# Performance work log

Measured on AMD Instinct MI355X. Metric: run time of the kernel, lower is better.

Reference implementation:

```python
import jax, jax.numpy as jnp
import numpy as np

PRIOR = 0.1      # prior_prob
P_NOISE = 0.05   # p
DAMPING = 0.5
BETA = 0.3
EPS = 1e-10


def compute_likelihood(Y_edges, prod_fail_others, beta_edges, p):
    p_sick_if_healthy = 1.0 - prod_fail_others
    p_sick_if_infected = 1.0 - prod_fail_others * (1.0 - beta_edges)
    normal_if_sick = (1.0 - p) * p_sick_if_healthy
    sick_if_sick = (1.0 - p) * p_sick_if_infected
    normal_if_normal = p * p_sick_if_healthy + (1.0 - p_sick_if_healthy)
    sick_if_normal = p * p_sick_if_infected + (1.0 - p_sick_if_infected)
    is_pos = Y_edges == 1
    L0 = jnp.where(is_pos, normal_if_sick, normal_if_normal)
    L1 = jnp.where(is_pos, sick_if_sick, sick_if_normal)
    return L0, L1


def setup_inputs() -> dict:
    key = jax.random.key(0)
    k1, k2, k3 = jax.random.split(key, 3)
    num_tests = 100000
    num_patients = 200000
    num_edges = 12800000
    Y_obs = jax.random.randint(k1, (num_tests,), 0, 2, dtype=jnp.int32)
    idx_i = jax.random.randint(k2, (num_edges,), 0, num_tests, dtype=jnp.int32)
    idx_j = jax.random.randint(k3, (num_edges,), 0, num_patients, dtype=jnp.int32)
    # beta_edges = 1.0 on diagonal entries, beta elsewhere (as in __init__)
    beta_edges = jnp.where(idx_i == idx_j, 1.0, BETA).astype(jnp.float32)
    return {"Y_obs": Y_obs, "idx_i": idx_i, "idx_j": idx_j,
            "beta_edges": beta_edges, "max_iters": 50,
            "num_patients": num_patients}


def reference(Y_obs, idx_i, idx_j, beta_edges, max_iters, num_patients):
    num_tests = Y_obs.shape[0]
    num_edges = idx_i.shape[0]
    Y_edges = Y_obs[idx_i]  # [E]

    def step(carry, it):
        msg_j_to_i, old0, old1, _ = carry
        # test-side aggregation: prob all other patients failed to infect test i
        fail = 1.0 - beta_edges * msg_j_to_i
        log_fail = jnp.log(fail + EPS)
        tot_log_fail = jax.ops.segment_sum(log_fail, idx_i, num_segments=num_tests)
        prod_fail_others = jnp.exp(tot_log_fail[idx_i]) / (fail + EPS)
        new0, new1 = compute_likelihood(Y_edges, prod_fail_others, beta_edges, P_NOISE)
        first = it == 0
        m0 = jnp.where(first, new0, DAMPING * new0 + (1.0 - DAMPING) * old0)
        m1 = jnp.where(first, new1, DAMPING * new1 + (1.0 - DAMPING) * old1)
        old0_n, old1_n = m0, m1  # stored BEFORE normalization, as in torch code
        norm = m0 + m1 + EPS
        log_m0 = jnp.log(m0 / norm + EPS)
        log_m1 = jnp.log(m1 / norm + EPS)
        # patient-side aggregation
        t0 = jax.ops.segment_sum(log_m0, idx_j, num_segments=num_patients)
        t1 = jax.ops.segment_sum(log_m1, idx_j, num_segments=num_patients)
        log_b0 = jnp.log(1.0 - PRIOR) + t0
        log_b1 = jnp.log(PRIOR) + t1
        beliefs = jax.nn.sigmoid(log_b1 - log_b0)  # = 1/(1+exp(lb0-lb1))
        msg_next = jax.nn.sigmoid((log_b1[idx_j] - log_m1) - (log_b0[idx_j] - log_m0))
        return (msg_next, old0_n, old1_n, beliefs), None

    init = (jnp.full((num_edges,), PRIOR, dtype=jnp.float32),
            jnp.zeros((num_edges,), jnp.float32),
            jnp.zeros((num_edges,), jnp.float32),
            jnp.full((num_patients,), PRIOR, dtype=jnp.float32))
    (_, _, _, node_beliefs), _ = jax.lax.scan(step, init, jnp.arange(max_iters))
    return node_beliefs
```

## Files before the change

### kernel.cpp

```cpp
#include <hip/hip_runtime.h>
#include <hip/hip_fp16.h>

#define EPSF   1e-10f
#define PRIORF 0.1f
#define QF     0.95f
#define BETAF  0.3f
#define BS     256
#define WPB    4
#define CAPT   4
#define LOGIT_PRIOR (-2.1972245773362196f)
#define GSH    13
#define NG_MAX 32
#define SPAN_I 256
#define NB2_MAX 1024
#define SPAN_J 128
#define NBJ_MAX 2048
#define CHA    16384
#define CHJ    32768
#define D16    0x2000u
#define JL16   0x1FFFu
#define NXCD   8
#define BLK_SL 2048

__device__ __forceinline__ float wave_sum(float v) {
    #pragma unroll
    for (int m = 32; m >= 1; m >>= 1) v += __shfl_xor(v, m, 64);
    return v;
}
__device__ __forceinline__ float frcp(float x) {
    return __builtin_amdgcn_rcpf(x);
}
__device__ __forceinline__ float calcD(float2 o) {
    float inv = frcp(o.x + o.y + EPSF);
    return __logf(o.y * inv + EPSF) - __logf(o.x * inv + EPSF);
}
__device__ __forceinline__ float sigmoidf(float x) {
    return frcp(1.0f + __expf(-x));
}
__device__ __forceinline__ float2 unpack(__half2 h) {
    return make_float2(__low2float(h), __high2float(h));
}

__device__ __forceinline__ int run_search(int cum, int len, int v0,
                                          int cidx, int NG, int* gout) {
    int lo = 0, hi = NG - 1;
    #pragma unroll
    for (int st = 0; st < 5; ++st) {
        int mid = (lo + hi) >> 1;
        int cmid = __shfl(cum, mid);
        int open = (lo < hi);
        int p = (cmid > cidx);
        int nhi = p ? mid : hi;
        int nlo = p ? lo : (mid + 1);
        hi = open ? nhi : hi;
        lo = open ? nlo : lo;
    }
    int cl = __shfl(cum, lo);
    int ll = __shfl(len, lo);
    int vv = __shfl(v0, lo);
    *gout = lo;
    return vv + cidx - (cl - ll);
}

__global__ __launch_bounds__(BS) void k_test(
    const int*            __restrict__ rowptrG,
    const unsigned short* __restrict__ jidx16,
    const int*            __restrict__ Y,
    const float*          __restrict__ delta,
    __half2*              __restrict__ oldm,
    int T, int NG, int first)
{
    int lane = threadIdx.x & 63;
    int i = blockIdx.x * WPB + (threadIdx.x >> 6);
    if (i >= T) return;
    int v0 = 0, v1 = 0;
    if (lane < NG) v0 = rowptrG[(size_t)i * NG + lane];
    int l2 = lane - 32;
    if (l2 >= 0 && l2 < NG) v1 = rowptrG[(size_t)(i + 1) * NG + l2];
    int endv = __shfl(v1, 32 + lane);
    int len = (lane < NG) ? (endv - v0) : 0;
    int cum = len;
    #pragma unroll
    for (int off = 1; off < 64; off <<= 1) {
        int t = __shfl_up(cum, off);
        if (lane >= off) cum += t;
    }
    int deg = __shfl(cum, 63);
    int nch = (deg + 63) >> 6;
    int ypos = (Y[i] == 1);
    float lsum = 0.0f;

    if (deg <= 64 * CAPT) {
        int ssv[CAPT]; int ksv[CAPT]; float2 osv[CAPT]; float fsv[CAPT];
        #pragma unroll
        for (int c = 0; c < CAPT; ++c) {
            if (c >= nch) break;
            int idx = c * 64 + lane;
            int cidx = min(idx, deg - 1);
            int g;
            int s = run_search(cum, len, v0, cidx, NG, &g);
            bool act = (idx < deg);
            int k = 0; float2 o = make_float2(0.f, 0.f); float f = 1.0f;
            if (act) {
                k = jidx16[s];
                float b = (k & D16) ? 1.0f : BETAF;
                float msg;
                if (first) msg = PRIORF;
                else {
                    o = unpack(oldm[s]);
                    int j = (g << GSH) | (k & JL16);
                    msg = sigmoidf(delta[j] - calcD(o));
                }
                f = 1.0f - b * msg;
                lsum += __logf(f + EPSF);
            }
            ssv[c] = act ? s : -1; ksv[c] = k; osv[c] = o; fsv[c] = f;
        }
        float Etot = __expf(wave_sum(lsum));
        #pragma unroll
        for (int c = 0; c < CAPT; ++c) {
            if (c >= nch) break;
            int s = ssv[c];
            if (s < 0) continue;
            int k = ksv[c]; float f = fsv[c];
            float b = (k & D16) ? 1.0f : BETAF;
            float prod = Etot * frcp(f + EPSF);
            float psh = 1.0f - prod;
            float psi = 1.0f - prod * (1.0f - b);
            float L0 = ypos ? QF * psh : 1.0f - QF * psh;
            float L1 = ypos ? QF * psi : 1.0f - QF * psi;
            float m0, m1;
            if (first) { m0 = L0; m1 = L1; }
            else { float2 o = osv[c]; m0 = 0.5f * L0 + 0.5f * o.x;
                                      m1 = 0.5f * L1 + 0.5f * o.y; }
            oldm[s] = __floats2half2_rn(m0, m1);
        }
    } else {
        for (int base = 0; base < deg; base += 64) {
            int idx = base + lane;
            int cidx = min(idx, deg - 1);
            int g;
            int s = run_search(cum, len, v0, cidx, NG, &g);
            if (idx < deg) {
                int k = jidx16[s];
                float b = (k & D16) ? 1.0f : BETAF;
                float msg;
                if (first) msg = PRIORF;
                else {
                    int j = (g << GSH) | (k & JL16);
                    msg = sigmoidf(delta[j] - calcD(unpack(oldm[s])));
                }
                lsum += __logf(1.0f - b * msg + EPSF);
            }
        }
        float Etot = __expf(wave_sum(lsum));
        for (int base = 0; base < deg; base += 64) {
            int idx = base + lane;
            int cidx = min(idx, deg - 1);
            int g;
            int s = run_search(cum, len, v0, cidx, NG, &g);
            if (idx < deg) {
                int k = jidx16[s];
                float b = (k & D16) ? 1.0f : BETAF;
                float2 o = make_float2(0.f, 0.f);
                float msg;
                if (first) msg = PRIORF;
                else { o = unpack(oldm[s]);
                       int j = (g << GSH) | (k & JL16);
                       msg = sigmoidf(delta[j] - calcD(o)); }
                float f = 1.0f - b * msg;
                float prod = Etot * frcp(f + EPSF);
                float psh = 1.0f - prod;
                float psi = 1.0f - prod * (1.0f - b);
                float L0 = ypos ? QF * psh : 1.0f - QF * psh;
                float L1 = ypos ? QF * psi : 1.0f - QF * psi;
                float m0, m1;
                if (first) { m0 = L0; m1 = L1; }
                else { m0 = 0.5f * L0 + 0.5f * o.x; m1 = 0.5f * L1 + 0.5f * o.y; }
                oldm[s] = __floats2half2_rn(m0, m1);
            }
        }
    }
}

__global__ __launch_bounds__(BS) void k_patient(
    const int*     __restrict__ colptr,
    const int*     __restrict__ eposJ,
    const __half2* __restrict__ oldm,
    float*         __restrict__ delta,
    float*         __restrict__ out, int P, int NG)
{
    int b = blockIdx.x;
    int x = b & (NXCD - 1);
    int r = b >> 3;
    int m = r / BLK_SL;
    int w = r % BLK_SL;
    int g = x + NXCD * m;
    if (g >= NG) return;
    int lane = threadIdx.x & 63;
    int p = (g << GSH) + w * WPB + (threadIdx.x >> 6);
    if (p >= P) return;
    int u0 = colptr[p], u1 = colptr[p + 1];
    float S = 0.0f;
    for (int u = u0 + lane; u < u1; u += 64)
        S += calcD(unpack(oldm[eposJ[u]]));
    S = wave_sum(S);
    if (lane == 0) {
        float d = LOGIT_PRIOR + S;
        delta[p] = d;
        out[p] = sigmoidf(d);
    }
}

__global__ void k_zf2(int* frontG, int* front2, int* frontJ,
                      int NG, int nb2tot, int nbj) {
    int t = blockIdx.x * blockDim.x + threadIdx.x;
    if (t <= NG) frontG[t] = 0;
    if (t <= nb2tot) front2[t] = 0;
    if (t <= nbj) frontJ[t] = 0;
}

__global__ __launch_bounds__(BS) void k_binG(
    const int* __restrict__ idx_i, const int* __restrict__ idx_j,
    int* __restrict__ frontG, unsigned* __restrict__ stageA,
    int E, int NG, int capA)
{
    __shared__ int h[NG_MAX], rsv[NG_MAX], cu[NG_MAX];
    int tid = threadIdx.x;
    if (tid < NG) h[tid] = 0;
    __syncthreads();
    int start = blockIdx.x * CHA, end = min(start + CHA, E);
    for (int e = start + tid; e < end; e += BS)
        atomicAdd(&h[idx_j[e] >> GSH], 1);
    __syncthreads();
    if (tid < NG) { int c = h[tid];
        rsv[tid] = c ? atomicAdd(&frontG[tid], c) : 0; cu[tid] = 0; }
    __syncthreads();
    for (int e = start + tid; e < end; e += BS) {
        int i = idx_i[e], j = idx_j[e];
        int g = j >> GSH;
        int pos = rsv[g] + atomicAdd(&cu[g], 1);
        if (pos < capA)
            stageA[(size_t)g * capA + pos] =
                ((unsigned)i << 14) | ((unsigned)(i == j) << 13)
                | (unsigned)(j & ((1 << GSH) - 1));
    }
}

__global__ __launch_bounds__(BS) void k_binI2(
    const unsigned* __restrict__ stageA, const int* __restrict__ frontG,
    int* __restrict__ front2, unsigned* __restrict__ stage2,
    int NG, int NB2, int capA, int cap2, int chunks)
{
    int g = blockIdx.x / chunks, c = blockIdx.x % chunks;
    int n = min(frontG[g], capA);
    int start = c * 2 * CHA, end = min(start + 2 * CHA, n);
    if (start >= end) return;
    __shared__ int h[NB2_MAX], rsv[NB2_MAX], cu[NB2_MAX];
    int tid = threadIdx.x;
    for (int b = tid; b < NB2; b += BS) h[b] = 0;
    __syncthreads();
    const unsigned* rb = stageA + (size_t)g * capA;
    for (int r = start + tid; r < end; r += BS)
        atomicAdd(&h[(rb[r] >> 14) >> 8], 1);
    __syncthreads();
    for (int b = tid; b < NB2; b += BS) {
        int cc = h[b];
        rsv[b] = cc ? atomicAdd(&front2[g * NB2 + b], cc) : 0;
        cu[b] = 0;
    }
    __syncthreads();
    for (int r = start + tid; r < end; r += BS) {
        unsigned v = rb[r];
        int i = (int)(v >> 14);
        int ib = i >> 8;
        int pos = rsv[ib] + atomicAdd(&cu[ib], 1);
        if (pos < cap2)
            stage2[(size_t)(g * NB2 + ib) * cap2 + pos] =
                ((unsigned)(i & 255) << 14) | (v & 0x3FFFu);
    }
}

__global__ void k_scan_front(int* a, int n, int cap) {
    __shared__ int tmp[BS];
    __shared__ int carry;
    int tid = threadIdx.x;
    if (tid == 0) carry = 0;
    __syncthreads();
    for (int base = 0; base < n; base += BS) {
        int i = base + tid;
        int v = (i < n) ? min(a[i], cap) : 0;
        tmp[tid] = v; __syncthreads();
        for (int off = 1; off < BS; off <<= 1) {
            int x = (tid >= off) ? tmp[tid - off] : 0;
            __syncthreads();
            tmp[tid] += x;
            __syncthreads();
        }
        int c = carry;
        if (i < n) a[i] = c + tmp[tid] - v;
        __syncthreads();
        if (tid == BS - 1) carry = c + tmp[tid];
        __syncthreads();
    }
    if (tid == 0) a[n] = carry;
}

__global__ __launch_bounds__(BS) void k_csr2(
    const unsigned* __restrict__ stage2, const int* __restrict__ front2s,
    int* __restrict__ rowptrG, unsigned short* __restrict__ jidx16,
    int T, int NG, int NB2, int cap2)
{
    __shared__ int deg[SPAN_I], loff[SPAN_I], cu[SPAN_I];
    int b = blockIdx.x, tid = threadIdx.x;
    int g = b / NB2, ib = b % NB2;
    int base = front2s[b];
    int n = min(front2s[b + 1] - base, cap2);
    deg[tid] = 0;
    __syncthreads();
    const unsigned* rb = stage2 + (size_t)b * cap2;
    for (int r = tid; r < n; r += BS)
        atomicAdd(&deg[rb[r] >> 14], 1);
    __syncthreads();
    loff[tid] = deg[tid];
    __syncthreads();
    for (int off = 1; off < SPAN_I; off <<= 1) {
        int v = (tid >= off) ? loff[tid - off] : 0;
        __syncthreads();
        loff[tid] += v;
        __syncthreads();
    }
    {
        int excl = loff[tid] - deg[tid];
        int i = ib * SPAN_I + tid;
        if (i < T) rowptrG[(size_t)i * NG + g] = base + excl;
        cu[tid] = base + excl;
    }
    __syncthreads();
    for (int r = tid; r < n; r += BS) {
        unsigned v = rb[r];
        int pos = atomicAdd(&cu[v >> 14], 1);
        jidx16[pos] = (unsigned short)(v & 0x3FFFu);
    }
}

__global__ void k_fin(const int* front2s, int* rowptrG, int T, int NG, int NB2) {
    int g = threadIdx.x;
    if (g < NG) rowptrG[(size_t)T * NG + g] = front2s[(g + 1) * NB2];
}

__global__ __launch_bounds__(BS) void k_binJ(
    const unsigned short* __restrict__ jidx16,
    const int* __restrict__ front2s,
    int* __restrict__ front, unsigned int* __restrict__ stage,
    int E, int nbj, int cap, int NG, int NB2)
{
    __shared__ int h[NBJ_MAX], rsv[NBJ_MAX], cu[NBJ_MAX];
    __shared__ int ends[NG_MAX];
    int tid = threadIdx.x;
    if (tid < NG) ends[tid] = front2s[(tid + 1) * NB2];
    for (int b = tid; b < nbj; b += BS) h[b] = 0;
    __syncthreads();
    int start = blockIdx.x * CHJ, end = min(start + CHJ, E);
    for (int e = start + tid; e < end; e += BS) {
        int lo = 0, hi = NG - 1;
        while (lo < hi) { int mid = (lo + hi) >> 1;
                          if (e < ends[mid]) hi = mid; else lo = mid + 1; }
        int j = (lo << GSH) | (jidx16[e] & JL16);
        atomicAdd(&h[j >> 7], 1);
    }
    __syncthreads();
    for (int b = tid; b < nbj; b += BS) {
        int c = h[b];
        rsv[b] = c ? atomicAdd(&front[b], c) : 0;
        cu[b] = 0;
    }
    __syncthreads();
    for (int e = start + tid; e < end; e += BS) {
        int lo = 0, hi = NG - 1;
        while (lo < hi) { int mid = (lo + hi) >> 1;
                          if (e < ends[mid]) hi = mid; else lo = mid + 1; }
        int j = (lo << GSH) | (jidx16[e] & JL16);
        int bb = j >> 7;
        int pos = rsv[bb] + atomicAdd(&cu[bb], 1);
        if (pos < cap)
            stage[(size_t)bb * cap + pos] = ((unsigned)(j & 127) << 24) | (unsigned)e;
    }
}

__global__ __launch_bounds__(BS) void k_csrJ(
    const unsigned int* __restrict__ stage, const int* __restrict__ fbase,
    int* __restrict__ colptr, int* __restrict__ eposJ, int P, int E, int cap)
{
    __shared__ int deg[SPAN_J], loff[SPAN_J], cu[SPAN_J];
    int b = blockIdx.x, tid = threadIdx.x;
    int gbase = fbase[b];
    int n = min(fbase[b + 1] - gbase, cap);
    if (tid < SPAN_J) deg[tid] = 0;
    __syncthreads();
    const unsigned int* rb = stage + (size_t)b * cap;
    for (int r = tid; r < n; r += BS)
        atomicAdd(&deg[rb[r] >> 24], 1);
    __syncthreads();
    if (tid < SPAN_J) loff[tid] = deg[tid];
    __syncthreads();
    for (int off = 1; off < SPAN_J; off <<= 1) {
        int v = 0;
        if (tid < SPAN_J && tid >= off) v = loff[tid - off];
        __syncthreads();
        if (tid < SPAN_J) loff[tid] += v;
        __syncthreads();
    }
    if (tid < SPAN_J) {
        int excl = loff[tid] - deg[tid];
        int p = b * SPAN_J + tid;
        if (p < P) colptr[p] = gbase + excl;
        cu[tid] = gbase + excl;
    }
    __syncthreads();
    for (int r = tid; r < n; r += BS) {
        unsigned int v = rb[r];
        int pos = atomicAdd(&cu[v >> 24], 1);
        eposJ[pos] = (int)(v & 0xFFFFFFu);
    }
    if (b == 0 && tid == 0) colptr[P] = E;
}

extern "C" void kernel_launch(void* const* d_in, const int* in_sizes, int n_in,
                              void* d_out, int out_size, void* d_ws, size_t ws_size,
                              hipStream_t stream) {
    const int* Y     = (const int*)d_in[0];
    const int* idx_i = (const int*)d_in[1];
    const int* idx_j = (const int*)d_in[2];
    const int T = in_sizes[0];
    const int E = in_sizes[1];
    const int P = out_size;
    const int ITERS = 50;

    int* eposJ = (int*)d_in[3];

    const int NG     = (P + (1 << GSH) - 1) >> GSH;
    const int NB2    = (T + SPAN_I - 1) / SPAN_I;
    const int nb2tot = NG * NB2;
    const int nbj    = (P + SPAN_J - 1) / SPAN_J;
    long long meanA = (long long)E * (1 << GSH) / P;
    const int capA  = (int)(meanA + (meanA >> 6) + 4096);
    long long mean2 = meanA * SPAN_I / T;
    const int cap2  = (int)(mean2 + (mean2 >> 4) + 256);
    const int capJ  = E / nbj + E / (nbj * 8) + 1024;

    char* ws = (char*)d_ws;
    auto alloc = [&](size_t bytes) -> char* {
        char* p = ws; ws += (bytes + 255) & ~(size_t)255; return p;
    };
    int* rowptrG = (int*)alloc((size_t)(T + 1) * NG * 4);
    int* colptr  = (int*)alloc((size_t)(P + 1) * 4);
    int* frontG  = (int*)alloc((size_t)(NG + 1) * 4);
    int* front2  = (int*)alloc((size_t)(nb2tot + 1) * 4);
    int* frontJ  = (int*)alloc((size_t)(nbj + 1) * 4);
    size_t szA = (size_t)capA * NG * 4, szjx = (size_t)E * 2;
    char* regionA = alloc(szA > szjx ? szA : szjx);
    unsigned*       stageA = (unsigned*)regionA;
    unsigned short* jidx16 = (unsigned short*)regionA;
    size_t oldm_b = ((size_t)E * 4 + 255) & ~(size_t)255;
    size_t sz2 = (size_t)cap2 * nb2tot * 4;
    size_t szJ = (size_t)capJ * nbj * 4;
    size_t szO = oldm_b + (size_t)P * 4;
    size_t szB = sz2 > szJ ? sz2 : szJ; if (szO > szB) szB = szO;
    char* regionB = alloc(szB);
    unsigned* stage2 = (unsigned*)regionB;
    unsigned* stageJ = (unsigned*)regionB;
    __half2*  oldm   = (__half2*)regionB;
    float*    delta  = (float*)(regionB + oldm_b);
    float*    out    = (float*)d_out;

    const int zb = (nb2tot + BS) / BS + 1;
    const int chunks = (capA + 2 * CHA - 1) / (2 * CHA);
    k_zf2<<<zb, BS, 0, stream>>>(frontG, front2, frontJ, NG, nb2tot, nbj);
    k_binG<<<(E + CHA - 1) / CHA, BS, 0, stream>>>(idx_i, idx_j, frontG, stageA,
                                                   E, NG, capA);
    k_binI2<<<NG * chunks, BS, 0, stream>>>(stageA, frontG, front2, stage2,
                                            NG, NB2, capA, cap2, chunks);
    k_scan_front<<<1, BS, 0, stream>>>(front2, nb2tot, cap2);
    k_csr2<<<nb2tot, BS, 0, stream>>>(stage2, front2, rowptrG, jidx16,
                                      T, NG, NB2, cap2);
    k_fin<<<1, 64, 0, stream>>>(front2, rowptrG, T, NG, NB2);
    k_binJ<<<(E + CHJ - 1) / CHJ, BS, 0, stream>>>(jidx16, front2, frontJ, stageJ,
                                                   E, nbj, capJ, NG, NB2);
    k_scan_front<<<1, BS, 0, stream>>>(frontJ, nbj, capJ);
    k_csrJ<<<nbj, BS, 0, stream>>>(stageJ, frontJ, colptr, eposJ, P, E, capJ);

    const int tgrid = (T + WPB - 1) / WPB;
    const int maxm  = (NG + NXCD - 1) / NXCD;
    const int pgrid = NXCD * maxm * BLK_SL;
    for (int it = 0; it < ITERS; ++it) {
        k_test<<<tgrid, BS, 0, stream>>>(rowptrG, jidx16, Y, delta, oldm,
                                         T, NG, it == 0);
        k_patient<<<pgrid, BS, 0, stream>>>(colptr, eposJ, oldm, delta, out,
                                            P, NG);
    }
}
```

Before: 9.546 ms.

## Precompute compact per-test edge streams to drop per-iteration run search

Adds a one-time preprocessing pass that builds a compact per-test row pointer and two edge streams. One stream packs the group and edge slot, the other holds the 16-bit patient index. The test kernel then reads these streams directly instead of rebuilding offsets from a per-group rowptr with a wave scan and binary search every iteration. The patient kernel moves to 1024-thread blocks with 16 waves each, and a binning chunk size is reduced. The cost is extra preprocessing kernels, about 6 bytes of stream storage per edge, and a workspace layout that reuses overlapping buffers.

```diff
diff --git a/kernel.cpp b/kernel.cpp
--- a/kernel.cpp
+++ b/kernel.cpp
@@ -16,11 +16,13 @@
 #define SPAN_J 128
 #define NBJ_MAX 2048
 #define CHA    16384
-#define CHJ    32768
+#define CHJ    8192
 #define D16    0x2000u
 #define JL16   0x1FFFu
 #define NXCD   8
-#define BLK_SL 2048
+#define BSP    1024
+#define WPBP   16
+#define BLK_SLP 512
 
 __device__ __forceinline__ float wave_sum(float v) {
     #pragma unroll
@@ -30,15 +32,15 @@
 __device__ __forceinline__ float frcp(float x) {
     return __builtin_amdgcn_rcpf(x);
 }
+__device__ __forceinline__ float2 unpack(__half2 h) {
+    return make_float2(__low2float(h), __high2float(h));
+}
 __device__ __forceinline__ float calcD(float2 o) {
     float inv = frcp(o.x + o.y + EPSF);
     return __logf(o.y * inv + EPSF) - __logf(o.x * inv + EPSF);
 }
 __device__ __forceinline__ float sigmoidf(float x) {
     return frcp(1.0f + __expf(-x));
-}
-__device__ __forceinline__ float2 unpack(__half2 h) {
-    return make_float2(__low2float(h), __high2float(h));
 }
 
 __device__ __forceinline__ int run_search(int cum, int len, int v0,
@@ -63,12 +65,332 @@
 }
 
 __global__ __launch_bounds__(BS) void k_test(
-    const int*            __restrict__ rowptrG,
-    const unsigned short* __restrict__ jidx16,
+    const int*            __restrict__ rowptrC,
+    const unsigned*       __restrict__ strmA,
+    const unsigned short* __restrict__ strmB,
     const int*            __restrict__ Y,
     const float*          __restrict__ delta,
     __half2*              __restrict__ oldm,
-    int T, int NG, int first)
+    int T, int first)
+{
+    int lane = threadIdx.x & 63;
+    int i = blockIdx.x * WPB + (threadIdx.x >> 6);
+    if (i >= T) return;
+    int r0 = rowptrC[i];
+    int deg = rowptrC[i + 1] - r0;
+    int nch = (deg + 63) >> 6;
+    int ypos = (Y[i] == 1);
+    float lsum = 0.0f;
+
+    if (deg <= 64 * CAPT) {
+        unsigned av[CAPT]; int kv[CAPT]; float2 ov[CAPT]; float fv[CAPT];
+        #pragma unroll
+        for (int c = 0; c < CAPT; ++c) {
+            if (c >= nch) break;
+            int idx = c * 64 + lane;
+            int q = r0 + min(idx, deg - 1);
+            unsigned a = strmA[q];
+            int k = strmB[q];
+            bool act = (idx < deg);
+            float2 o = make_float2(0.f, 0.f);
+            float b = (k & D16) ? 1.0f : BETAF;
+            float msg;
+            if (first) msg = PRIORF;
+            else {
+                int s = (int)(a & 0xFFFFFFu);
+                o = unpack(oldm[s]);
+                int j = ((int)(a >> 24) << GSH) | (k & JL16);
+                msg = sigmoidf(delta[j] - calcD(o));
+            }
+            float f = 1.0f - b * msg;
+            if (act) lsum += __logf(f + EPSF);
+            av[c] = a; kv[c] = k; ov[c] = o; fv[c] = f;
+        }
+        float Etot = __expf(wave_sum(lsum));
+        #pragma unroll
+        for (int c = 0; c < CAPT; ++c) {
+            if (c >= nch) break;
+            int idx = c * 64 + lane;
+            if (idx >= deg) continue;
+            int k = kv[c]; float f = fv[c];
+            float b = (k & D16) ? 1.0f : BETAF;
+            float prod = Etot * frcp(f + EPSF);
+            float psh = 1.0f - prod;
+            float psi = 1.0f - prod * (1.0f - b);
+            float L0 = ypos ? QF * psh : 1.0f - QF * psh;
+            float L1 = ypos ? QF * psi : 1.0f - QF * psi;
+            float m0, m1;
+            if (first) { m0 = L0; m1 = L1; }
+            else { m0 = 0.5f * L0 + 0.5f * ov[c].x;
+                   m1 = 0.5f * L1 + 0.5f * ov[c].y; }
+            int s = (int)(av[c] & 0xFFFFFFu);
+            oldm[s] = __floats2half2_rn(m0, m1);
+        }
+    } else {
+        for (int base = 0; base < deg; base += 64) {
+            int idx = base + lane;
+            int q = r0 + min(idx, deg - 1);
+            unsigned a = strmA[q];
+            int k = strmB[q];
+            float b = (k & D16) ? 1.0f : BETAF;
+            float msg;
+            if (first) msg = PRIORF;
+            else {
+                int s = (int)(a & 0xFFFFFFu);
+                int j = ((int)(a >> 24) << GSH) | (k & JL16);
+                msg = sigmoidf(delta[j] - calcD(unpack(oldm[s])));
+            }
+            if (idx < deg) lsum += __logf(1.0f - b * msg + EPSF);
+        }
+        float Etot = __expf(wave_sum(lsum));
+        for (int base = 0; base < deg; base += 64) {
+            int idx = base + lane;
+            int q = r0 + min(idx, deg - 1);
+            unsigned a = strmA[q];
+            int k = strmB[q];
+            float b = (k & D16) ? 1.0f : BETAF;
+            int s = (int)(a & 0xFFFFFFu);
+            float2 o = make_float2(0.f, 0.f);
+            float msg;
+            if (first) msg = PRIORF;
+            else {
+                o = unpack(oldm[s]);
+                int j = ((int)(a >> 24) << GSH) | (k & JL16);
+                msg = sigmoidf(delta[j] - calcD(o));
+            }
+            float f = 1.0f - b * msg;
+            float prod = Etot * frcp(f + EPSF);
+            float psh = 1.0f - prod;
+            float psi = 1.0f - prod * (1.0f - b);
+            float L0 = ypos ? QF * psh : 1.0f - QF * psh;
+            float L1 = ypos ? QF * psi : 1.0f - QF * psi;
+            float m0, m1;
+            if (first) { m0 = L0; m1 = L1; }
+            else { m0 = 0.5f * L0 + 0.5f * o.x; m1 = 0.5f * L1 + 0.5f * o.y; }
+            if (idx < deg) oldm[s] = __floats2half2_rn(m0, m1);
+        }
+    }
+}
+
+__global__ __launch_bounds__(BSP) void k_patient(
+    const int*     __restrict__ colptr,
+    const int*     __restrict__ eposJ,
+    const __half2* __restrict__ oldm,
+    float*         __restrict__ delta,
+    float*         __restrict__ out, int P, int NG)
+{
+    int b = blockIdx.x;
+    int x = b & (NXCD - 1);
+    int r = b >> 3;
+    int m = r >> 9;
+    int w = r & (BLK_SLP - 1);
+    int g = x + NXCD * m;
+    if (g >= NG) return;
+    int lane = threadIdx.x & 63;
+    int p = (g << GSH) + w * WPBP + (threadIdx.x >> 6);
+    if (p >= P) return;
+    int u0 = colptr[p], u1 = colptr[p + 1];
+    float S = 0.0f;
+    for (int u = u0 + lane; u < u1; u += 64)
+        S += calcD(unpack(oldm[eposJ[u]]));
+    S = wave_sum(S);
+    if (lane == 0) {
+        float d = LOGIT_PRIOR + S;
+        delta[p] = d;
+        out[p] = sigmoidf(d);
+    }
+}
+
+__global__ void k_zf2(int* frontG, int* front2, int* frontJ,
+                      int NG, int nb2tot, int nbj) {
+    int t = blockIdx.x * blockDim.x + threadIdx.x;
+    if (t <= NG) frontG[t] = 0;
+    if (t <= nb2tot) front2[t] = 0;
+    if (t <= nbj) frontJ[t] = 0;
+}
+
+__global__ __launch_bounds__(BS) void k_binG(
+    const int* __restrict__ idx_i, const int* __restrict__ idx_j,
+    int* __restrict__ frontG, unsigned* __restrict__ stageA,
+    int E, int NG, int capA)
+{
+    __shared__ int h[NG_MAX], rsv[NG_MAX], cu[NG_MAX];
+    int tid = threadIdx.x;
+    if (tid < NG) h[tid] = 0;
+    __syncthreads();
+    int start = blockIdx.x * CHA, end = min(start + CHA, E);
+    for (int e = start + tid; e < end; e += BS)
+        atomicAdd(&h[idx_j[e] >> GSH], 1);
+    __syncthreads();
+    if (tid < NG) { int c = h[tid];
+        rsv[tid] = c ? atomicAdd(&frontG[tid], c) : 0; cu[tid] = 0; }
+    __syncthreads();
+    for (int e = start + tid; e < end; e += BS) {
+        int i = idx_i[e], j = idx_j[e];
+        int g = j >> GSH;
+        int pos = rsv[g] + atomicAdd(&cu[g], 1);
+        if (pos < capA)
+            stageA[(size_t)g * capA + pos] =
+                ((unsigned)i << 14) | ((unsigned)(i == j) << 13)
+                | (unsigned)(j & ((1 << GSH) - 1));
+    }
+}
+
+__global__ __launch_bounds__(BS) void k_binI2(
+    const unsigned* __restrict__ stageA, const int* __restrict__ frontG,
+    int* __restrict__ front2, unsigned* __restrict__ stage2,
+    int NG, int NB2, int capA, int cap2, int chunks)
+{
+    int g = blockIdx.x / chunks, c = blockIdx.x % chunks;
+    int n = min(frontG[g], capA);
+    int start = c * 2 * CHA, end = min(start + 2 * CHA, n);
+    if (start >= end) return;
+    __shared__ int h[NB2_MAX], rsv[NB2_MAX], cu[NB2_MAX];
+    int tid = threadIdx.x;
+    for (int b = tid; b < NB2; b += BS) h[b] = 0;
+    __syncthreads();
+    const unsigned* rb = stageA + (size_t)g * capA;
+    for (int r = start + tid; r < end; r += BS)
+        atomicAdd(&h[(rb[r] >> 14) >> 8], 1);
+    __syncthreads();
+    for (int b = tid; b < NB2; b += BS) {
+        int cc = h[b];
+        rsv[b] = cc ? atomicAdd(&front2[g * NB2 + b], cc) : 0;
+        cu[b] = 0;
+    }
+    __syncthreads();
+    for (int r = start + tid; r < end; r += BS) {
+        unsigned v = rb[r];
+        int i = (int)(v >> 14);
+        int ib = i >> 8;
+        int pos = rsv[ib] + atomicAdd(&cu[ib], 1);
+        if (pos < cap2)
+            stage2[(size_t)(g * NB2 + ib) * cap2 + pos] =
+                ((unsigned)(i & 255) << 14) | (v & 0x3FFFu);
+    }
+}
+
+__global__ void k_scan_front(int* a, int n, int cap) {
+    __shared__ int tmp[BS];
+    __shared__ int carry;
+    int tid = threadIdx.x;
+    if (tid == 0) carry = 0;
+    __syncthreads();
+    for (int base = 0; base < n; base += BS) {
+        int i = base + tid;
+        int v = (i < n) ? min(a[i], cap) : 0;
+        tmp[tid] = v; __syncthreads();
+        for (int off = 1; off < BS; off <<= 1) {
+            int x = (tid >= off) ? tmp[tid - off] : 0;
+            __syncthreads();
+            tmp[tid] += x;
+            __syncthreads();
+        }
+        int c = carry;
+        if (i < n) a[i] = c + tmp[tid] - v;
+        __syncthreads();
+        if (tid == BS - 1) carry = c + tmp[tid];
+        __syncthreads();
+    }
+    if (tid == 0) a[n] = carry;
+}
+
+__global__ __launch_bounds__(BS) void k_csr2(
+    const unsigned* __restrict__ stage2, const int* __restrict__ front2s,
+    int* __restrict__ rowptrG, unsigned short* __restrict__ jidx16,
+    int T, int NG, int NB2, int cap2)
+{
+    __shared__ int deg[SPAN_I], loff[SPAN_I], cu[SPAN_I];
+    int b = blockIdx.x, tid = threadIdx.x;
+    int g = b / NB2, ib = b % NB2;
+    int base = front2s[b];
+    int n = min(front2s[b + 1] - base, cap2);
+    deg[tid] = 0;
+    __syncthreads();
+    const unsigned* rb = stage2 + (size_t)b * cap2;
+    for (int r = tid; r < n; r += BS)
+        atomicAdd(&deg[rb[r] >> 14], 1);
+    __syncthreads();
+    loff[tid] = deg[tid];
+    __syncthreads();
+    for (int off = 1; off < SPAN_I; off <<= 1) {
+        int v = (tid >= off) ? loff[tid - off] : 0;
+        __syncthreads();
+        loff[tid] += v;
+        __syncthreads();
+    }
+    {
+        int excl = loff[tid] - deg[tid];
+        int i = ib * SPAN_I + tid;
+        if (i < T) rowptrG[(size_t)i * NG + g] = base + excl;
+        cu[tid] = base + excl;
+    }
+    __syncthreads();
+    for (int r = tid; r < n; r += BS) {
+        unsigned v = rb[r];
+        int pos = atomicAdd(&cu[v >> 14], 1);
+        jidx16[pos] = (unsigned short)(v & 0x3FFFu);
+    }
+}
+
+__global__ void k_fin(const int* front2s, int* rowptrG, int T, int NG, int NB2) {
+    int g = threadIdx.x;
+    if (g < NG) rowptrG[(size_t)T * NG + g] = front2s[(g + 1) * NB2];
+}
+
+__global__ __launch_bounds__(BS) void k_degrow(
+    const int* __restrict__ rowptrG, int* __restrict__ cnt, int T, int NG)
+{
+    int i = blockIdx.x * BS + threadIdx.x;
+    if (i >= T) return;
+    int d = 0;
+    for (int g = 0; g < NG; ++g)
+        d += rowptrG[(size_t)(i + 1) * NG + g] - rowptrG[(size_t)i * NG + g];
+    cnt[i] = d;
+}
+
+__global__ __launch_bounds__(BS) void k_scan_part(
+    const int* __restrict__ in, int* __restrict__ aux, int n)
+{
+    __shared__ int t[BS];
+    int b = blockIdx.x, tid = threadIdx.x;
+    int i = b * BS + tid;
+    int v = (i < n) ? in[i] : 0;
+    t[tid] = v; __syncthreads();
+    for (int off = 1; off < BS; off <<= 1) {
+        int x = (tid >= off) ? t[tid - off] : 0;
+        __syncthreads();
+        t[tid] += x;
+        __syncthreads();
+    }
+    if (tid == BS - 1) aux[b] = t[tid];
+}
+__global__ __launch_bounds__(BS) void k_scan_fin(
+    const int* __restrict__ in, const int* __restrict__ aux,
+    int* __restrict__ out, int n, int nblk)
+{
+    __shared__ int t[BS];
+    int b = blockIdx.x, tid = threadIdx.x;
+    int i = b * BS + tid;
+    int v = (i < n) ? in[i] : 0;
+    t[tid] = v; __syncthreads();
+    for (int off = 1; off < BS; off <<= 1) {
+        int x = (tid >= off) ? t[tid - off] : 0;
+        __syncthreads();
+        t[tid] += x;
+        __syncthreads();
+    }
+    if (i < n) out[i] = aux[b] + t[tid] - v;
+    if (b == 0 && tid == 0) out[n] = aux[nblk];
+}
+
+__global__ __launch_bounds__(BS) void k_mkrow(
+    const int*            __restrict__ rowptrG,
+    const unsigned short* __restrict__ jidx16,
+    const int*            __restrict__ rowptrC,
+    unsigned*             __restrict__ strmA,
+    unsigned short*       __restrict__ strmB,
+    int T, int NG)
 {
     int lane = threadIdx.x & 63;
     int i = blockIdx.x * WPB + (threadIdx.x >> 6);
@@ -86,267 +408,18 @@
         if (lane >= off) cum += t;
     }
     int deg = __shfl(cum, 63);
-    int nch = (deg + 63) >> 6;
-    int ypos = (Y[i] == 1);
-    float lsum = 0.0f;
-
-    if (deg <= 64 * CAPT) {
-        int ssv[CAPT]; int ksv[CAPT]; float2 osv[CAPT]; float fsv[CAPT];
-        #pragma unroll
-        for (int c = 0; c < CAPT; ++c) {
-            if (c >= nch) break;
-            int idx = c * 64 + lane;
-            int cidx = min(idx, deg - 1);
-            int g;
-            int s = run_search(cum, len, v0, cidx, NG, &g);
-            bool act = (idx < deg);
-            int k = 0; float2 o = make_float2(0.f, 0.f); float f = 1.0f;
-            if (act) {
-                k = jidx16[s];
-                float b = (k & D16) ? 1.0f : BETAF;
-                float msg;
-                if (first) msg = PRIORF;
-                else {
-                    o = unpack(oldm[s]);
-                    int j = (g << GSH) | (k & JL16);
-                    msg = sigmoidf(delta[j] - calcD(o));
-                }
-                f = 1.0f - b * msg;
-                lsum += __logf(f + EPSF);
-            }
-            ssv[c] = act ? s : -1; ksv[c] = k; osv[c] = o; fsv[c] = f;
+    int r0 = rowptrC[i];
+    for (int base = 0; base < deg; base += 64) {
+        int idx = base + lane;
+        int cidx = min(idx, deg - 1);
+        int g;
+        int s = run_search(cum, len, v0, cidx, NG, &g);
+        if (idx < deg) {
+            int q = r0 + idx;
+            strmA[q] = ((unsigned)g << 24) | (unsigned)s;
+            strmB[q] = jidx16[s];
         }
-        float Etot = __expf(wave_sum(lsum));
-        #pragma unroll
-        for (int c = 0; c < CAPT; ++c) {
-            if (c >= nch) break;
-            int s = ssv[c];
-            if (s < 0) continue;
-            int k = ksv[c]; float f = fsv[c];
-            float b = (k & D16) ? 1.0f : BETAF;
-            float prod = Etot * frcp(f + EPSF);
-            float psh = 1.0f - prod;
-            float psi = 1.0f - prod * (1.0f - b);
-            float L0 = ypos ? QF * psh : 1.0f - QF * psh;
-            float L1 = ypos ? QF * psi : 1.0f - QF * psi;
-            float m0, m1;
-            if (first) { m0 = L0; m1 = L1; }
-            else { float2 o = osv[c]; m0 = 0.5f * L0 + 0.5f * o.x;
-                                      m1 = 0.5f * L1 + 0.5f * o.y; }
-            oldm[s] = __floats2half2_rn(m0, m1);
-        }
-    } else {
-        for (int base = 0; base < deg; base += 64) {
-            int idx = base + lane;
-            int cidx = min(idx, deg - 1);
-            int g;
-            int s = run_search(cum, len, v0, cidx, NG, &g);
-            if (idx < deg) {
-                int k = jidx16[s];
-                float b = (k & D16) ? 1.0f : BETAF;
-                float msg;
-                if (first) msg = PRIORF;
-                else {
-                    int j = (g << GSH) | (k & JL16);
-                    msg = sigmoidf(delta[j] - calcD(unpack(oldm[s])));
-                }
-                lsum += __logf(1.0f - b * msg + EPSF);
-            }
-        }
-        float Etot = __expf(wave_sum(lsum));
-        for (int base = 0; base < deg; base += 64) {
-            int idx = base + lane;
-            int cidx = min(idx, deg - 1);
-            int g;
-            int s = run_search(cum, len, v0, cidx, NG, &g);
-            if (idx < deg) {
-                int k = jidx16[s];
-                float b = (k & D16) ? 1.0f : BETAF;
-                float2 o = make_float2(0.f, 0.f);
-                float msg;
-                if (first) msg = PRIORF;
-                else { o = unpack(oldm[s]);
-                       int j = (g << GSH) | (k & JL16);
-                       msg = sigmoidf(delta[j] - calcD(o)); }
-                float f = 1.0f - b * msg;
-                float prod = Etot * frcp(f + EPSF);
-                float psh = 1.0f - prod;
-                float psi = 1.0f - prod * (1.0f - b);
-                float L0 = ypos ? QF * psh : 1.0f - QF * psh;
-                float L1 = ypos ? QF * psi : 1.0f - QF * psi;
-                float m0, m1;
-                if (first) { m0 = L0; m1 = L1; }
-                else { m0 = 0.5f * L0 + 0.5f * o.x; m1 = 0.5f * L1 + 0.5f * o.y; }
-                oldm[s] = __floats2half2_rn(m0, m1);
-            }
-        }
-    }
-}
-
-__global__ __launch_bounds__(BS) void k_patient(
-    const int*     __restrict__ colptr,
-    const int*     __restrict__ eposJ,
-    const __half2* __restrict__ oldm,
-    float*         __restrict__ delta,
-    float*         __restrict__ out, int P, int NG)
-{
-    int b = blockIdx.x;
-    int x = b & (NXCD - 1);
-    int r = b >> 3;
-    int m = r / BLK_SL;
-    int w = r % BLK_SL;
-    int g = x + NXCD * m;
-    if (g >= NG) return;
-    int lane = threadIdx.x & 63;
-    int p = (g << GSH) + w * WPB + (threadIdx.x >> 6);
-    if (p >= P) return;
-    int u0 = colptr[p], u1 = colptr[p + 1];
-    float S = 0.0f;
-    for (int u = u0 + lane; u < u1; u += 64)
-        S += calcD(unpack(oldm[eposJ[u]]));
-    S = wave_sum(S);
-    if (lane == 0) {
-        float d = LOGIT_PRIOR + S;
-        delta[p] = d;
-        out[p] = sigmoidf(d);
-    }
-}
-
-__global__ void k_zf2(int* frontG, int* front2, int* frontJ,
-                      int NG, int nb2tot, int nbj) {
-    int t = blockIdx.x * blockDim.x + threadIdx.x;
-    if (t <= NG) frontG[t] = 0;
-    if (t <= nb2tot) front2[t] = 0;
-    if (t <= nbj) frontJ[t] = 0;
-}
-
-__global__ __launch_bounds__(BS) void k_binG(
-    const int* __restrict__ idx_i, const int* __restrict__ idx_j,
-    int* __restrict__ frontG, unsigned* __restrict__ stageA,
-    int E, int NG, int capA)
-{
-    __shared__ int h[NG_MAX], rsv[NG_MAX], cu[NG_MAX];
-    int tid = threadIdx.x;
-    if (tid < NG) h[tid] = 0;
-    __syncthreads();
-    int start = blockIdx.x * CHA, end = min(start + CHA, E);
-    for (int e = start + tid; e < end; e += BS)
-        atomicAdd(&h[idx_j[e] >> GSH], 1);
-    __syncthreads();
-    if (tid < NG) { int c = h[tid];
-        rsv[tid] = c ? atomicAdd(&frontG[tid], c) : 0; cu[tid] = 0; }
-    __syncthreads();
-    for (int e = start + tid; e < end; e += BS) {
-        int i = idx_i[e], j = idx_j[e];
-        int g = j >> GSH;
-        int pos = rsv[g] + atomicAdd(&cu[g], 1);
-        if (pos < capA)
-            stageA[(size_t)g * capA + pos] =
-                ((unsigned)i << 14) | ((unsigned)(i == j) << 13)
-                | (unsigned)(j & ((1 << GSH) - 1));
-    }
-}
-
-__global__ __launch_bounds__(BS) void k_binI2(
-    const unsigned* __restrict__ stageA, const int* __restrict__ frontG,
-    int* __restrict__ front2, unsigned* __restrict__ stage2,
-    int NG, int NB2, int capA, int cap2, int chunks)
-{
-    int g = blockIdx.x / chunks, c = blockIdx.x % chunks;
-    int n = min(frontG[g], capA);
-    int start = c * 2 * CHA, end = min(start + 2 * CHA, n);
-    if (start >= end) return;
-    __shared__ int h[NB2_MAX], rsv[NB2_MAX], cu[NB2_MAX];
-    int tid = threadIdx.x;
-    for (int b = tid; b < NB2; b += BS) h[b] = 0;
-    __syncthreads();
-    const unsigned* rb = stageA + (size_t)g * capA;
-    for (int r = start + tid; r < end; r += BS)
-        atomicAdd(&h[(rb[r] >> 14) >> 8], 1);
-    __syncthreads();
-    for (int b = tid; b < NB2; b += BS) {
-        int cc = h[b];
-        rsv[b] = cc ? atomicAdd(&front2[g * NB2 + b], cc) : 0;
-        cu[b] = 0;
-    }
-    __syncthreads();
-    for (int r = start + tid; r < end; r += BS) {
-        unsigned v = rb[r];
-        int i = (int)(v >> 14);
-        int ib = i >> 8;
-        int pos = rsv[ib] + atomicAdd(&cu[ib], 1);
-        if (pos < cap2)
-            stage2[(size_t)(g * NB2 + ib) * cap2 + pos] =
-                ((unsigned)(i & 255) << 14) | (v & 0x3FFFu);
-    }
-}
-
-__global__ void k_scan_front(int* a, int n, int cap) {
-    __shared__ int tmp[BS];
-    __shared__ int carry;
-    int tid = threadIdx.x;
-    if (tid == 0) carry = 0;
-    __syncthreads();
-    for (int base = 0; base < n; base += BS) {
-        int i = base + tid;
-        int v = (i < n) ? min(a[i], cap) : 0;
-        tmp[tid] = v; __syncthreads();
-        for (int off = 1; off < BS; off <<= 1) {
-            int x = (tid >= off) ? tmp[tid - off] : 0;
-            __syncthreads();
-            tmp[tid] += x;
-            __syncthreads();
-        }
-        int c = carry;
-        if (i < n) a[i] = c + tmp[tid] - v;
-        __syncthreads();
-        if (tid == BS - 1) carry = c + tmp[tid];
-        __syncthreads();
-    }
-    if (tid == 0) a[n] = carry;
-}
-
-__global__ __launch_bounds__(BS) void k_csr2(
-    const unsigned* __restrict__ stage2, const int* __restrict__ front2s,
-    int* __restrict__ rowptrG, unsigned short* __restrict__ jidx16,
-    int T, int NG, int NB2, int cap2)
-{
-    __shared__ int deg[SPAN_I], loff[SPAN_I], cu[SPAN_I];
-    int b = blockIdx.x, tid = threadIdx.x;
-    int g = b / NB2, ib = b % NB2;
-    int base = front2s[b];
-    int n = min(front2s[b + 1] - base, cap2);
-    deg[tid] = 0;
-    __syncthreads();
-    const unsigned* rb = stage2 + (size_t)b * cap2;
-    for (int r = tid; r < n; r += BS)
-        atomicAdd(&deg[rb[r] >> 14], 1);
-    __syncthreads();
-    loff[tid] = deg[tid];
-    __syncthreads();
-    for (int off = 1; off < SPAN_I; off <<= 1) {
-        int v = (tid >= off) ? loff[tid - off] : 0;
-        __syncthreads();
-        loff[tid] += v;
-        __syncthreads();
-    }
-    {
-        int excl = loff[tid] - deg[tid];
-        int i = ib * SPAN_I + tid;
-        if (i < T) rowptrG[(size_t)i * NG + g] = base + excl;
-        cu[tid] = base + excl;
-    }
-    __syncthreads();
-    for (int r = tid; r < n; r += BS) {
-        unsigned v = rb[r];
-        int pos = atomicAdd(&cu[v >> 14], 1);
-        jidx16[pos] = (unsigned short)(v & 0x3FFFu);
-    }
-}
-
-__global__ void k_fin(const int* front2s, int* rowptrG, int T, int NG, int NB2) {
-    int g = threadIdx.x;
-    if (g < NG) rowptrG[(size_t)T * NG + g] = front2s[(g + 1) * NB2];
+    }
 }
 
 __global__ __launch_bounds__(BS) void k_binJ(
@@ -443,36 +516,36 @@
     const int NB2    = (T + SPAN_I - 1) / SPAN_I;
     const int nb2tot = NG * NB2;
     const int nbj    = (P + SPAN_J - 1) / SPAN_J;
+    const int NBLK   = (T + BS - 1) / BS;
     long long meanA = (long long)E * (1 << GSH) / P;
     const int capA  = (int)(meanA + (meanA >> 6) + 4096);
     long long mean2 = meanA * SPAN_I / T;
     const int cap2  = (int)(mean2 + (mean2 >> 4) + 256);
     const int capJ  = E / nbj + E / (nbj * 8) + 1024;
 
-    char* ws = (char*)d_ws;
-    auto alloc = [&](size_t bytes) -> char* {
-        char* p = ws; ws += (bytes + 255) & ~(size_t)255; return p;
+    char* base = (char*)d_ws;
+    size_t sz2 = (size_t)cap2 * nb2tot * 4;
+    unsigned*       strmA  = (unsigned*)base;
+    unsigned short* strmB  = (unsigned short*)(base + (size_t)E * 4);
+    __half2*        oldm   = (__half2*)(base + (size_t)E * 6);
+    unsigned*       stage2 = (unsigned*)base;
+    unsigned*       stageA = (unsigned*)(base + ((sz2 + 255) & ~(size_t)255));
+    unsigned short* jidx16 = (unsigned short*)(base + (size_t)E * 6);
+    int*            rowptrG= (int*)(base + (size_t)E * 8);
+    unsigned*       stageJ = (unsigned*)base;
+    size_t o = (size_t)E * 10;
+    auto sub = [&](size_t bytes) -> char* {
+        char* p = base + o; o += (bytes + 255) & ~(size_t)255; return p;
     };
-    int* rowptrG = (int*)alloc((size_t)(T + 1) * NG * 4);
-    int* colptr  = (int*)alloc((size_t)(P + 1) * 4);
-    int* frontG  = (int*)alloc((size_t)(NG + 1) * 4);
-    int* front2  = (int*)alloc((size_t)(nb2tot + 1) * 4);
-    int* frontJ  = (int*)alloc((size_t)(nbj + 1) * 4);
-    size_t szA = (size_t)capA * NG * 4, szjx = (size_t)E * 2;
-    char* regionA = alloc(szA > szjx ? szA : szjx);
-    unsigned*       stageA = (unsigned*)regionA;
-    unsigned short* jidx16 = (unsigned short*)regionA;
-    size_t oldm_b = ((size_t)E * 4 + 255) & ~(size_t)255;
-    size_t sz2 = (size_t)cap2 * nb2tot * 4;
-    size_t szJ = (size_t)capJ * nbj * 4;
-    size_t szO = oldm_b + (size_t)P * 4;
-    size_t szB = sz2 > szJ ? sz2 : szJ; if (szO > szB) szB = szO;
-    char* regionB = alloc(szB);
-    unsigned* stage2 = (unsigned*)regionB;
-    unsigned* stageJ = (unsigned*)regionB;
-    __half2*  oldm   = (__half2*)regionB;
-    float*    delta  = (float*)(regionB + oldm_b);
-    float*    out    = (float*)d_out;
+    int*   colptr  = (int*)sub((size_t)(P + 1) * 4);
+    int*   rowptrC = (int*)sub((size_t)(T + 1) * 4);
+    float* delta   = (float*)sub((size_t)P * 4);
+    int*   cnt     = (int*)sub((size_t)T * 4);
+    int*   auxS    = (int*)sub((size_t)(NBLK + 2) * 4);
+    int*   frontG  = (int*)sub((size_t)(NG + 1) * 4);
+    int*   front2  = (int*)sub((size_t)(nb2tot + 1) * 4);
+    int*   frontJ  = (int*)sub((size_t)(nbj + 1) * 4);
+    float* out     = (float*)d_out;
 
     const int zb = (nb2tot + BS) / BS + 1;
     const int chunks = (capA + 2 * CHA - 1) / (2 * CHA);
@@ -485,18 +558,24 @@
     k_csr2<<<nb2tot, BS, 0, stream>>>(stage2, front2, rowptrG, jidx16,
                                       T, NG, NB2, cap2);
     k_fin<<<1, 64, 0, stream>>>(front2, rowptrG, T, NG, NB2);
+    k_degrow<<<NBLK, BS, 0, stream>>>(rowptrG, cnt, T, NG);
+    k_scan_part<<<NBLK, BS, 0, stream>>>(cnt, auxS, T);
+    k_scan_front<<<1, BS, 0, stream>>>(auxS, NBLK, 0x7FFFFFFF);
+    k_scan_fin<<<NBLK, BS, 0, stream>>>(cnt, auxS, rowptrC, T, NBLK);
     k_binJ<<<(E + CHJ - 1) / CHJ, BS, 0, stream>>>(jidx16, front2, frontJ, stageJ,
                                                    E, nbj, capJ, NG, NB2);
     k_scan_front<<<1, BS, 0, stream>>>(frontJ, nbj, capJ);
     k_csrJ<<<nbj, BS, 0, stream>>>(stageJ, frontJ, colptr, eposJ, P, E, capJ);
-
     const int tgrid = (T + WPB - 1) / WPB;
+    k_mkrow<<<tgrid, BS, 0, stream>>>(rowptrG, jidx16, rowptrC, strmA, strmB,
+                                      T, NG);
+
     const int maxm  = (NG + NXCD - 1) / NXCD;
-    const int pgrid = NXCD * maxm * BLK_SL;
+    const int pgrid = NXCD * maxm * BLK_SLP;
     for (int it = 0; it < ITERS; ++it) {
-        k_test<<<tgrid, BS, 0, stream>>>(rowptrG, jidx16, Y, delta, oldm,
-                                         T, NG, it == 0);
-        k_patient<<<pgrid, BS, 0, stream>>>(colptr, eposJ, oldm, delta, out,
-                                            P, NG);
-    }
-}
+        k_test<<<tgrid, BS, 0, stream>>>(rowptrC, strmA, strmB, Y, delta, oldm,
+                                         T, it == 0);
+        k_patient<<<pgrid, BSP, 0, stream>>>(colptr, eposJ, oldm, delta, out,
+                                             P, NG);
+    }
+}
```

After: 9.697 ms. About the same (+1.6%).
